# Kernel optimization log

Measured on AMD Instinct MI355X. Metric: run time of the kernel, lower is better.

The kernel has to match this reference:

```python
import jax, jax.numpy as jnp
import numpy as np

C_IN = 32
C_OUT = 32


def setup_inputs() -> dict:
    key = jax.random.key(0)
    k1, k2, k3 = jax.random.split(key, 3)
    B, N, P_DIM = 32, 4096, 64
    X = jax.random.normal(k1, (B, N, C_IN), dtype=jnp.float32)
    P = jax.random.normal(k2, (B, N, P_DIM), dtype=jnp.float32)
    # glorot-ish scale for the hypernetwork Dense kernel (p_dim -> c_in*c_out)
    scale = (2.0 / (P_DIM + C_IN * C_OUT)) ** 0.5
    Wk = jax.random.normal(k3, (P_DIM, C_IN * C_OUT), dtype=jnp.float32) * scale
    return {"X": X, "P": P, "Wk": Wk}


def reference(X, P, Wk):
    B, N, c_in = X.shape
    # hypernetwork: per-position weight generation  [B,N,p] @ [p, c_in*c_out]
    A = jnp.einsum('bnp,pq->bnq', P, Wk)
    W = A.reshape(B, N, c_in, C_OUT)          # [B,N,c_in,c_out]
    W = jax.nn.relu(W)                        # sigma(W)
    # batched per-position GEMV: y_bno = sum_i X_bni * W_bnio
    out = jnp.einsum('bni,bnio->bno', X, W)   # [B,N,c_out]
    return out
```

## Files before the change

### kernel.cpp

```cpp
#include <hip/hip_runtime.h>

#define CI 32
#define CO 32
#define PD 64
#define QDIM 1024
#define M_TOTAL (32*4096)
#define TILE_M 128
#define NBLK (M_TOTAL/TILE_M)
#define WG_THREADS 256
#define XLS 33
#define OLS 33

typedef float  f32x2  __attribute__((ext_vector_type(2)));
typedef float  f32x4  __attribute__((ext_vector_type(4)));
typedef float  f32x16 __attribute__((ext_vector_type(16)));
typedef __bf16 bf16x4 __attribute__((ext_vector_type(4)));
typedef __bf16 bf16x8 __attribute__((ext_vector_type(8)));

__global__ __launch_bounds__(256)
void wk_pack_kernel(const float* __restrict__ Wk, __bf16* __restrict__ wsF)
{
    __shared__ float tile[64][33];
    const int q0 = blockIdx.x * 32;
    const int t  = threadIdx.x;
#pragma unroll
    for (int s = 0; s < 2; ++s) {
        const int idx = t + s * 256;
        const int k = idx >> 3, ch = idx & 7;
        f32x4 v = *(const f32x4*)(Wk + (size_t)k * QDIM + q0 + ch * 4);
        tile[k][ch*4+0] = v[0]; tile[k][ch*4+1] = v[1];
        tile[k][ch*4+2] = v[2]; tile[k][ch*4+3] = v[3];
    }
    __syncthreads();
    const int qq = t >> 3;
    const int g  = t & 7;
    bf16x8 o;
#pragma unroll
    for (int j = 0; j < 8; ++j) o[j] = (__bf16)tile[g*8 + j][qq];
    *(bf16x8*)(wsF + (size_t)blockIdx.x * 2048 + g * 256 + qq * 8) = o;
}

__global__ __launch_bounds__(WG_THREADS, 2)
void cond_dense_kernel(const float* __restrict__ Xg, const float* __restrict__ Pg,
                       const __bf16* __restrict__ wsF, float* __restrict__ outg)
{
    __shared__ union {
        __bf16 p[TILE_M * PD];
        float  o[2 * 64 * OLS];
    } U;
    __shared__ float Xl[TILE_M * XLS];

    const int t   = threadIdx.x;
    const int l   = t & 63;
    const int w   = t >> 6;
    const int rg  = w & 1;
    const int ih  = w >> 1;
    const int l31 = l & 31;
    const int hi  = l >> 5;
    const int tile0 = blockIdx.x * TILE_M;
    const int m0  = rg * 64 + l31;

    {
        const float* Pb = Pg + (size_t)tile0 * PD;
#pragma unroll
        for (int s = 0; s < 8; ++s) {
            const int id = t + 256 * s;
            const int r = id >> 4, ch = id & 15;
            f32x4 v = *(const f32x4*)(Pb + (size_t)r * PD + ch * 4);
            bf16x4 bv;
#pragma unroll
            for (int j = 0; j < 4; ++j) bv[j] = (__bf16)v[j];
            char* dst = (char*)U.p + r * 128
                      + ((((ch >> 1) ^ (r & 7)) << 4) | ((ch & 1) * 8));
            *(bf16x4*)dst = bv;
        }
        const float* Xb = Xg + (size_t)tile0 * CI;
#pragma unroll
        for (int s = 0; s < 4; ++s) {
            const int id = t + 256 * s;
            const int r = id >> 3, ch = id & 7;
            f32x4 v = *(const f32x4*)(Xb + (size_t)r * CI + ch * 4);
#pragma unroll
            for (int j = 0; j < 4; ++j) Xl[r * XLS + ch * 4 + j] = v[j];
        }
    }
    __syncthreads();

    bf16x8 bfA[4], bfB[4];
#pragma unroll
    for (int kq = 0; kq < 4; ++kq) {
        const int g = ((kq * 2 + hi) ^ (l31 & 7)) << 4;
        bfA[kq] = *(const bf16x8*)((const char*)U.p + m0 * 128 + g);
        bfB[kq] = *(const bf16x8*)((const char*)U.p + (m0 + 32) * 128 + g);
    }

    f32x2 oA[8] = {}, oB[8] = {};
    const __bf16* abase = wsF + (size_t)(ih * 16) * 2048
                        + (size_t)hi * 256 + (size_t)l31 * 8;
    const float* xb0 = &Xl[m0 * XLS + ih * 16];
    const float* xb1 = &Xl[(m0 + 32) * XLS + ih * 16];

    bf16x8 a0[4], a1[4];
    auto aload = [&](int i, bf16x8* buf) {
        const __bf16* ap = abase + (size_t)i * 2048;
        buf[0] = *(const bf16x8*)(ap);
        buf[1] = *(const bf16x8*)(ap +  512);
        buf[2] = *(const bf16x8*)(ap + 1024);
        buf[3] = *(const bf16x8*)(ap + 1536);
    };
    const f32x2 zero2 = {0.0f, 0.0f};
    auto step = [&](const bf16x8* a, int i) {
        const float xl = xb0[i];
        const float xh = xb1[i];
        f32x16 c0 = {}, c1 = {};
#pragma unroll
        for (int kq = 0; kq < 4; ++kq) {
            c0 = __builtin_amdgcn_mfma_f32_32x32x16_bf16(a[kq], bfA[kq], c0, 0, 0, 0);
            c1 = __builtin_amdgcn_mfma_f32_32x32x16_bf16(a[kq], bfB[kq], c1, 0, 0, 0);
        }
        const f32x2 xl2 = {xl, xl}, xh2 = {xh, xh};
#pragma unroll
        for (int r = 0; r < 8; ++r) {
            f32x2 p0 = {c0[2*r], c0[2*r + 1]};
            f32x2 p1 = {c1[2*r], c1[2*r + 1]};
            oA[r] += __builtin_elementwise_max(p0, zero2) * xl2;
            oB[r] += __builtin_elementwise_max(p1, zero2) * xh2;
        }
    };

    aload(0, a0);
    aload(1, a1);
    for (int ii = 0; ii < 8; ++ii) {
        step(a0, 2 * ii);
        if (ii < 7) aload(2 * ii + 2, a0);
        step(a1, 2 * ii + 1);
        if (ii < 7) aload(2 * ii + 3, a1);
    }

    __syncthreads();
    if (ih == 1) {
        const int ob = (rg * 64 + l) * OLS;
#pragma unroll
        for (int r = 0; r < 8; ++r) {
            *(f32x2*)&U.o[ob + 2*r]      = oA[r];
            *(f32x2*)&U.o[ob + 16 + 2*r] = oB[r];
        }
    }
    __syncthreads();
    if (ih == 0) {
        const int ob = (rg * 64 + l) * OLS;
#pragma unroll
        for (int r = 0; r < 8; ++r) {
            oA[r] += *(const f32x2*)&U.o[ob + 2*r];
            oB[r] += *(const f32x2*)&U.o[ob + 16 + 2*r];
        }
        float* orow  = outg + (size_t)(tile0 + m0) * CO + 4 * hi;
        float* orow2 = orow + 32 * CO;
#pragma unroll
        for (int rq = 0; rq < 4; ++rq) {
            f32x4 vA, vB;
#pragma unroll
            for (int j = 0; j < 4; ++j) {
                vA[j] = oA[2*rq + (j >> 1)][j & 1];
                vB[j] = oB[2*rq + (j >> 1)][j & 1];
            }
            *(f32x4*)(orow  + 8 * rq) = vA;
            *(f32x4*)(orow2 + 8 * rq) = vB;
        }
    }
}

extern "C" void kernel_launch(void* const* d_in, const int* in_sizes, int n_in,
                              void* d_out, int out_size, void* d_ws, size_t ws_size,
                              hipStream_t stream)
{
    const float* X  = (const float*)d_in[0];
    const float* P  = (const float*)d_in[1];
    const float* Wk = (const float*)d_in[2];
    float* out  = (float*)d_out;
    __bf16* wsF = (__bf16*)d_ws;

    wk_pack_kernel<<<dim3(QDIM / 32), dim3(256), 0, stream>>>(Wk, wsF);
    cond_dense_kernel<<<dim3(NBLK), dim3(WG_THREADS), 0, stream>>>(X, P, wsF, out);
}
```

Baseline: 36.98 us.

## Fuse Wk packing into persistent kernel with LDS-resident bf16 weights

```diff
diff --git a/kernel.cpp b/kernel.cpp
--- a/kernel.cpp
+++ b/kernel.cpp
@@ -5,11 +5,11 @@
 #define PD 64
 #define QDIM 1024
 #define M_TOTAL (32*4096)
-#define TILE_M 128
-#define NBLK (M_TOTAL/TILE_M)
+#define TILE_M 256
+#define NBLK 256
+#define NTILES 2
 #define WG_THREADS 256
-#define XLS 33
-#define OLS 33
+#define LDS_BYTES 163840
 
 typedef float  f32x2  __attribute__((ext_vector_type(2)));
 typedef float  f32x4  __attribute__((ext_vector_type(4)));
@@ -17,143 +17,125 @@
 typedef __bf16 bf16x4 __attribute__((ext_vector_type(4)));
 typedef __bf16 bf16x8 __attribute__((ext_vector_type(8)));
 
-__global__ __launch_bounds__(256)
-void wk_pack_kernel(const float* __restrict__ Wk, __bf16* __restrict__ wsF)
+extern __shared__ char lds_raw[];
+
+__global__ __launch_bounds__(WG_THREADS, 1)
+void cond_fused(const float* __restrict__ Xg, const float* __restrict__ Pg,
+                const float* __restrict__ Wk, float* __restrict__ outg)
 {
-    __shared__ float tile[64][33];
-    const int q0 = blockIdx.x * 32;
-    const int t  = threadIdx.x;
-#pragma unroll
-    for (int s = 0; s < 2; ++s) {
-        const int idx = t + s * 256;
-        const int k = idx >> 3, ch = idx & 7;
-        f32x4 v = *(const f32x4*)(Wk + (size_t)k * QDIM + q0 + ch * 4);
-        tile[k][ch*4+0] = v[0]; tile[k][ch*4+1] = v[1];
-        tile[k][ch*4+2] = v[2]; tile[k][ch*4+3] = v[3];
-    }
-    __syncthreads();
-    const int qq = t >> 3;
-    const int g  = t & 7;
-    bf16x8 o;
-#pragma unroll
-    for (int j = 0; j < 8; ++j) o[j] = (__bf16)tile[g*8 + j][qq];
-    *(bf16x8*)(wsF + (size_t)blockIdx.x * 2048 + g * 256 + qq * 8) = o;
-}
-
-__global__ __launch_bounds__(WG_THREADS, 2)
-void cond_dense_kernel(const float* __restrict__ Xg, const float* __restrict__ Pg,
-                       const __bf16* __restrict__ wsF, float* __restrict__ outg)
-{
-    __shared__ union {
-        __bf16 p[TILE_M * PD];
-        float  o[2 * 64 * OLS];
-    } U;
-    __shared__ float Xl[TILE_M * XLS];
+    __bf16* Al = (__bf16*)lds_raw;
+    float*  Ux = (float*)(lds_raw + 131072);
+    __bf16* Up = (__bf16*)(lds_raw + 131072);
 
     const int t   = threadIdx.x;
     const int l   = t & 63;
     const int w   = t >> 6;
-    const int rg  = w & 1;
-    const int ih  = w >> 1;
     const int l31 = l & 31;
     const int hi  = l >> 5;
-    const int tile0 = blockIdx.x * TILE_M;
-    const int m0  = rg * 64 + l31;
+    const int m0  = w * 64 + l31;
 
-    {
+    f32x4 px[16], xx[8];
+    auto load_px = [&](int tile0) {
         const float* Pb = Pg + (size_t)tile0 * PD;
+        const float* Xb = Xg + (size_t)tile0 * CI;
+#pragma unroll
+        for (int s = 0; s < 16; ++s) {
+            const int id = t + 256 * s;
+            px[s] = *(const f32x4*)(Pb + (size_t)(id >> 4) * PD + (id & 15) * 4);
+        }
 #pragma unroll
         for (int s = 0; s < 8; ++s) {
             const int id = t + 256 * s;
-            const int r = id >> 4, ch = id & 15;
-            f32x4 v = *(const f32x4*)(Pb + (size_t)r * PD + ch * 4);
-            bf16x4 bv;
-#pragma unroll
-            for (int j = 0; j < 4; ++j) bv[j] = (__bf16)v[j];
-            char* dst = (char*)U.p + r * 128
-                      + ((((ch >> 1) ^ (r & 7)) << 4) | ((ch & 1) * 8));
-            *(bf16x4*)dst = bv;
-        }
-        const float* Xb = Xg + (size_t)tile0 * CI;
-#pragma unroll
-        for (int s = 0; s < 4; ++s) {
-            const int id = t + 256 * s;
-            const int r = id >> 3, ch = id & 7;
-            f32x4 v = *(const f32x4*)(Xb + (size_t)r * CI + ch * 4);
-#pragma unroll
-            for (int j = 0; j < 4; ++j) Xl[r * XLS + ch * 4 + j] = v[j];
-        }
-    }
-    __syncthreads();
-
-    bf16x8 bfA[4], bfB[4];
-#pragma unroll
-    for (int kq = 0; kq < 4; ++kq) {
-        const int g = ((kq * 2 + hi) ^ (l31 & 7)) << 4;
-        bfA[kq] = *(const bf16x8*)((const char*)U.p + m0 * 128 + g);
-        bfB[kq] = *(const bf16x8*)((const char*)U.p + (m0 + 32) * 128 + g);
-    }
-
-    f32x2 oA[8] = {}, oB[8] = {};
-    const __bf16* abase = wsF + (size_t)(ih * 16) * 2048
-                        + (size_t)hi * 256 + (size_t)l31 * 8;
-    const float* xb0 = &Xl[m0 * XLS + ih * 16];
-    const float* xb1 = &Xl[(m0 + 32) * XLS + ih * 16];
-
-    bf16x8 a0[4], a1[4];
-    auto aload = [&](int i, bf16x8* buf) {
-        const __bf16* ap = abase + (size_t)i * 2048;
-        buf[0] = *(const bf16x8*)(ap);
-        buf[1] = *(const bf16x8*)(ap +  512);
-        buf[2] = *(const bf16x8*)(ap + 1024);
-        buf[3] = *(const bf16x8*)(ap + 1536);
-    };
-    const f32x2 zero2 = {0.0f, 0.0f};
-    auto step = [&](const bf16x8* a, int i) {
-        const float xl = xb0[i];
-        const float xh = xb1[i];
-        f32x16 c0 = {}, c1 = {};
-#pragma unroll
-        for (int kq = 0; kq < 4; ++kq) {
-            c0 = __builtin_amdgcn_mfma_f32_32x32x16_bf16(a[kq], bfA[kq], c0, 0, 0, 0);
-            c1 = __builtin_amdgcn_mfma_f32_32x32x16_bf16(a[kq], bfB[kq], c1, 0, 0, 0);
-        }
-        const f32x2 xl2 = {xl, xl}, xh2 = {xh, xh};
-#pragma unroll
-        for (int r = 0; r < 8; ++r) {
-            f32x2 p0 = {c0[2*r], c0[2*r + 1]};
-            f32x2 p1 = {c1[2*r], c1[2*r + 1]};
-            oA[r] += __builtin_elementwise_max(p0, zero2) * xl2;
-            oB[r] += __builtin_elementwise_max(p1, zero2) * xh2;
+            xx[s] = *(const f32x4*)(Xb + (size_t)(id >> 3) * CI + (id & 7) * 4);
         }
     };
 
-    aload(0, a0);
-    aload(1, a1);
-    for (int ii = 0; ii < 8; ++ii) {
-        step(a0, 2 * ii);
-        if (ii < 7) aload(2 * ii + 2, a0);
-        step(a1, 2 * ii + 1);
-        if (ii < 7) aload(2 * ii + 3, a1);
+    const int base0 = blockIdx.x * TILE_M;
+    load_px(base0);
+
+    for (int k = 0; k < 64; ++k) {
+        f32x4 v = *(const f32x4*)(Wk + (size_t)k * QDIM + t * 4);
+#pragma unroll
+        for (int j = 0; j < 4; ++j) {
+            const int q = t * 4 + j;
+            Al[(q >> 5) * 2048 + (k >> 3) * 256 + (q & 31) * 8 + (k & 7)] = (__bf16)v[j];
+        }
     }
 
-    __syncthreads();
-    if (ih == 1) {
-        const int ob = (rg * 64 + l) * OLS;
+    for (int tt = 0; tt < NTILES; ++tt) {
+        const int tile0 = base0 + tt * (NBLK * TILE_M);
+        __syncthreads();
+
 #pragma unroll
-        for (int r = 0; r < 8; ++r) {
-            *(f32x2*)&U.o[ob + 2*r]      = oA[r];
-            *(f32x2*)&U.o[ob + 16 + 2*r] = oB[r];
+        for (int s = 0; s < 8; ++s) {
+            const int id = t + 256 * s;
+            const int r = id >> 3, ch = id & 7;
+#pragma unroll
+            for (int j = 0; j < 4; ++j) Ux[(ch * 4 + j) * 256 + r] = xx[s][j];
         }
-    }
-    __syncthreads();
-    if (ih == 0) {
-        const int ob = (rg * 64 + l) * OLS;
+        __syncthreads();
+        float x0[CI], x1[CI];
 #pragma unroll
-        for (int r = 0; r < 8; ++r) {
-            oA[r] += *(const f32x2*)&U.o[ob + 2*r];
-            oB[r] += *(const f32x2*)&U.o[ob + 16 + 2*r];
+        for (int i = 0; i < CI; ++i) {
+            x0[i] = Ux[i * 256 + m0];
+            x1[i] = Ux[i * 256 + m0 + 32];
         }
+        __syncthreads();
+#pragma unroll
+        for (int s = 0; s < 16; ++s) {
+            const int id = t + 256 * s;
+            const int r = id >> 4, ch = id & 15;
+            bf16x4 bv;
+#pragma unroll
+            for (int j = 0; j < 4; ++j) bv[j] = (__bf16)px[s][j];
+            *(bf16x4*)((char*)Up + r * 128
+                       + ((((ch >> 1) ^ (r & 7)) << 4) | ((ch & 1) * 8))) = bv;
+        }
+        if (tt + 1 < NTILES) load_px(base0 + (tt + 1) * (NBLK * TILE_M));
+        __syncthreads();
+        bf16x8 bfA[4], bfB[4];
+#pragma unroll
+        for (int kq = 0; kq < 4; ++kq) {
+            const int g = ((kq * 2 + hi) ^ (l31 & 7)) << 4;
+            bfA[kq] = *(const bf16x8*)((const char*)Up + m0 * 128 + g);
+            bfB[kq] = *(const bf16x8*)((const char*)Up + (m0 + 32) * 128 + g);
+        }
+
+        f32x2 oA[8] = {}, oB[8] = {};
+        const char* abase = (const char*)Al + hi * 512 + l31 * 16;
+        bf16x8 a0[4], a1[4];
+        auto aload = [&](int i, bf16x8* buf) {
+#pragma unroll
+            for (int c = 0; c < 4; ++c)
+                buf[c] = *(const bf16x8*)(abase + (size_t)i * 4096 + c * 1024);
+        };
+        const f32x2 zero2 = {0.0f, 0.0f};
+        auto stepf = [&](const bf16x8* a, float xl, float xh) {
+            f32x16 c0 = {}, c1 = {};
+#pragma unroll
+            for (int kq = 0; kq < 4; ++kq) {
+                c0 = __builtin_amdgcn_mfma_f32_32x32x16_bf16(a[kq], bfA[kq], c0, 0, 0, 0);
+                c1 = __builtin_amdgcn_mfma_f32_32x32x16_bf16(a[kq], bfB[kq], c1, 0, 0, 0);
+            }
+            const f32x2 xl2 = {xl, xl}, xh2 = {xh, xh};
+#pragma unroll
+            for (int r = 0; r < 8; ++r) {
+                f32x2 p0 = {c0[2*r], c0[2*r + 1]};
+                f32x2 p1 = {c1[2*r], c1[2*r + 1]};
+                oA[r] += __builtin_elementwise_max(p0, zero2) * xl2;
+                oB[r] += __builtin_elementwise_max(p1, zero2) * xh2;
+            }
+        };
+        aload(0, a0);
+        aload(1, a1);
+#pragma unroll
+        for (int ii = 0; ii < 16; ++ii) {
+            stepf(a0, x0[2*ii], x1[2*ii]);
+            if (ii < 15) aload(2*ii + 2, a0);
+            stepf(a1, x0[2*ii + 1], x1[2*ii + 1]);
+            if (ii < 15) aload(2*ii + 3, a1);
+        }
+
         float* orow  = outg + (size_t)(tile0 + m0) * CO + 4 * hi;
         float* orow2 = orow + 32 * CO;
 #pragma unroll
@@ -177,9 +159,9 @@
     const float* X  = (const float*)d_in[0];
     const float* P  = (const float*)d_in[1];
     const float* Wk = (const float*)d_in[2];
-    float* out  = (float*)d_out;
-    __bf16* wsF = (__bf16*)d_ws;
+    float* out = (float*)d_out;
 
-    wk_pack_kernel<<<dim3(QDIM / 32), dim3(256), 0, stream>>>(Wk, wsF);
-    cond_dense_kernel<<<dim3(NBLK), dim3(WG_THREADS), 0, stream>>>(X, P, wsF, out);
+    hipFuncSetAttribute((const void*)cond_fused,
+                        hipFuncAttributeMaxDynamicSharedMemorySize, LDS_BYTES);
+    cond_fused<<<dim3(NBLK), dim3(WG_THREADS), LDS_BYTES, stream>>>(X, P, Wk, out);
 }
```

Result: slower. 41.11 us (+11.2%).
